# Performance work log

Measured on AMD Instinct MI355X. Metric: run time of the kernel, lower is better.

The kernel has to match this reference:

```python
import jax, jax.numpy as jnp
import numpy as np
import math

D_MODEL = 1024
N_HEADS = 16
D_K = D_MODEL // N_HEADS
MAX_REL = 128


def setup_inputs() -> dict:
    key = jax.random.key(0)
    ks = jax.random.split(key, 10)
    B, S = 2, 2048
    std = 1.0 / math.sqrt(D_MODEL)
    inp = {
        "x": jax.random.normal(ks[0], (B, S, D_MODEL), dtype=jnp.float32),
        "Wq": jax.random.normal(ks[1], (D_MODEL, D_MODEL), dtype=jnp.float32) * std,
        "bq": jnp.zeros((D_MODEL,), dtype=jnp.float32),
        "Wk": jax.random.normal(ks[2], (D_MODEL, D_MODEL), dtype=jnp.float32) * std,
        "bk": jnp.zeros((D_MODEL,), dtype=jnp.float32),
        "Wv": jax.random.normal(ks[3], (D_MODEL, D_MODEL), dtype=jnp.float32) * std,
        "bv": jnp.zeros((D_MODEL,), dtype=jnp.float32),
        "Wo": jax.random.normal(ks[4], (D_MODEL, D_MODEL), dtype=jnp.float32) * std,
        "bo": jnp.zeros((D_MODEL,), dtype=jnp.float32),
        "rel_bias": jax.random.normal(ks[5], (N_HEADS, 2 * MAX_REL + 1), dtype=jnp.float32) * 0.02,
    }
    return inp


def _rel_bias_matrix(rel_bias, seq_len):
    # (H, S, S) gathered relative-position bias
    pos = jnp.arange(seq_len)
    rel = pos[:, None] - pos[None, :]
    idx = jnp.clip(rel, -MAX_REL, MAX_REL) + MAX_REL  # (S, S) in [0, 2M]
    return rel_bias[:, idx]  # (H, S, S)


def reference(x, Wq, bq, Wk, bk, Wv, bv, Wo, bo, rel_bias):
    B, S, _ = x.shape
    def proj(W, b):
        y = x @ W.T + b  # torch Linear: x @ W^T + b
        return y.reshape(B, S, N_HEADS, D_K).transpose(0, 2, 1, 3)  # (B,H,S,Dk)
    Q, K, V = proj(Wq, bq), proj(Wk, bk), proj(Wv, bv)
    scores = jnp.einsum("bhqd,bhkd->bhqk", Q, K) / math.sqrt(D_K)
    scores = scores + _rel_bias_matrix(rel_bias, S)[None]
    attn = jax.nn.softmax(scores, axis=-1)
    out = jnp.einsum("bhqk,bhkd->bhqd", attn, V)
    out = out.transpose(0, 2, 1, 3).reshape(B, S, D_MODEL)
    return out @ Wo.T + bo
```

## Files before the change

### kernel.cpp

```cpp
#include <hip/hip_runtime.h>

static constexpr int DM = 1024;
static constexpr int NH = 16;
static constexpr int DK = 64;
static constexpr int S  = 2048;
static constexpr int B  = 2;
static constexpr float LOG2E = 1.4426950408889634f;
static constexpr float FMAX  = 11.0f;

typedef _Float16 f16;
typedef _Float16 f16x8 __attribute__((ext_vector_type(8)));
typedef _Float16 f16x4 __attribute__((ext_vector_type(4)));
typedef float    f32x4 __attribute__((ext_vector_type(4)));

static constexpr size_t NX = (size_t)B * S * DM;
static constexpr size_t NW = (size_t)DM * DM;

__global__ __launch_bounds__(256) void cvt_f16(const float* __restrict__ x,
                                               const float* __restrict__ wq,
                                               const float* __restrict__ wk,
                                               const float* __restrict__ wv,
                                               const float* __restrict__ wo,
                                               f16* __restrict__ xh,
                                               f16* __restrict__ wqh,
                                               f16* __restrict__ wkh,
                                               f16* __restrict__ wvh,
                                               f16* __restrict__ woh)
{
    const size_t base = ((size_t)blockIdx.x * 256 + threadIdx.x) * 8;
    const float* src; f16* dst; size_t off;
    if (base < NX) { src = x; dst = xh; off = base; }
    else {
        const size_t rem = base - NX;
        const int seg = (int)(rem >> 20);
        off = rem & (NW - 1);
        src = seg == 0 ? wq : (seg == 1 ? wk : (seg == 2 ? wv : wo));
        dst = seg == 0 ? wqh : (seg == 1 ? wkh : (seg == 2 ? wvh : woh));
    }
    float4 a = *(const float4*)&src[off];
    float4 b = *(const float4*)&src[off + 4];
    f16x8 h = { (f16)a.x, (f16)a.y, (f16)a.z, (f16)a.w,
                (f16)b.x, (f16)b.y, (f16)b.z, (f16)b.w };
    *(f16x8*)&dst[off] = h;
}

template<int MODE>
__global__ __launch_bounds__(256) void gemm_h(const f16* __restrict__ A,
                                              const f16* __restrict__ W0,
                                              const f16* __restrict__ W1,
                                              const f16* __restrict__ W2,
                                              const float* __restrict__ b0,
                                              const float* __restrict__ b1,
                                              const float* __restrict__ b2,
                                              void* __restrict__ o0,
                                              void* __restrict__ o1,
                                              void* __restrict__ o2)
{
    __shared__ f16 As[128 * 72];
    __shared__ f16 Bs[128 * 72];

    const int t    = threadIdx.x;
    const int w    = t >> 6;
    const int lane = t & 63;
    const int tx   = lane & 15;
    const int quad = lane >> 4;
    const int wm   = w >> 1;
    const int wn   = w & 1;
    const int m0   = blockIdx.y * 128;

    const f16* W; const float* bias; f16* outh = nullptr; float* outf = nullptr;
    float scale; int n0;
    if (MODE == 0) {
        const int wsel = blockIdx.x >> 3;
        n0   = (blockIdx.x & 7) * 128;
        W    = wsel == 0 ? W0 : (wsel == 1 ? W1 : W2);
        bias = wsel == 0 ? b0 : (wsel == 1 ? b1 : b2);
        outh = (f16*)(wsel == 0 ? o0 : (wsel == 1 ? o1 : o2));
        scale = wsel == 0 ? LOG2E * 0.125f : 1.0f;
    } else {
        n0 = blockIdx.x * 128;
        W = W0; bias = b0; outf = (float*)o0; scale = 1.0f;
    }

    const int lr = t >> 2;
    const int lc = (t & 3) * 8;

    f32x4 acc[4][4];
#pragma unroll
    for (int mt = 0; mt < 4; ++mt)
#pragma unroll
        for (int nt = 0; nt < 4; ++nt) acc[mt][nt] = (f32x4){0.f, 0.f, 0.f, 0.f};

    f16x8 ga[4], gb[4];
    {
        const f16* Ap = A + (size_t)(m0 + lr) * DM + lc;
        const f16* Wp = W + (size_t)(n0 + lr) * DM + lc;
        ga[0] = *(const f16x8*)(Ap);
        ga[1] = *(const f16x8*)(Ap + 32);
        ga[2] = *(const f16x8*)(Ap + (size_t)64 * DM);
        ga[3] = *(const f16x8*)(Ap + (size_t)64 * DM + 32);
        gb[0] = *(const f16x8*)(Wp);
        gb[1] = *(const f16x8*)(Wp + 32);
        gb[2] = *(const f16x8*)(Wp + (size_t)64 * DM);
        gb[3] = *(const f16x8*)(Wp + (size_t)64 * DM + 32);
    }

    for (int k0 = 0; k0 < DM; k0 += 64) {
        __syncthreads();
        *(f16x8*)&As[ lr       * 72 + lc     ] = ga[0];
        *(f16x8*)&As[ lr       * 72 + lc + 32] = ga[1];
        *(f16x8*)&As[(lr + 64) * 72 + lc     ] = ga[2];
        *(f16x8*)&As[(lr + 64) * 72 + lc + 32] = ga[3];
        *(f16x8*)&Bs[ lr       * 72 + lc     ] = gb[0];
        *(f16x8*)&Bs[ lr       * 72 + lc + 32] = gb[1];
        *(f16x8*)&Bs[(lr + 64) * 72 + lc     ] = gb[2];
        *(f16x8*)&Bs[(lr + 64) * 72 + lc + 32] = gb[3];
        if (k0 + 64 < DM) {
            const f16* Ap = A + (size_t)(m0 + lr) * DM + k0 + 64 + lc;
            const f16* Wp = W + (size_t)(n0 + lr) * DM + k0 + 64 + lc;
            ga[0] = *(const f16x8*)(Ap);
            ga[1] = *(const f16x8*)(Ap + 32);
            ga[2] = *(const f16x8*)(Ap + (size_t)64 * DM);
            ga[3] = *(const f16x8*)(Ap + (size_t)64 * DM + 32);
            gb[0] = *(const f16x8*)(Wp);
            gb[1] = *(const f16x8*)(Wp + 32);
            gb[2] = *(const f16x8*)(Wp + (size_t)64 * DM);
            gb[3] = *(const f16x8*)(Wp + (size_t)64 * DM + 32);
        }
        __syncthreads();

        f16x8 af[4][2];
#pragma unroll
        for (int mt = 0; mt < 4; ++mt)
#pragma unroll
            for (int ks = 0; ks < 2; ++ks)
                af[mt][ks] = *(const f16x8*)&As[(wm*64 + mt*16 + tx)*72 + ks*32 + quad*8];
#pragma unroll
        for (int nt = 0; nt < 4; ++nt) {
#pragma unroll
            for (int ks = 0; ks < 2; ++ks) {
                f16x8 bf = *(const f16x8*)&Bs[(wn*64 + nt*16 + tx)*72 + ks*32 + quad*8];
#pragma unroll
                for (int mt = 0; mt < 4; ++mt)
                    acc[mt][nt] = __builtin_amdgcn_mfma_f32_16x16x32_f16(af[mt][ks], bf, acc[mt][nt], 0, 0, 0);
            }
        }
    }

#pragma unroll
    for (int nt = 0; nt < 4; ++nt) {
        const int n = n0 + wn*64 + nt*16 + tx;
        const float bn = bias[n];
#pragma unroll
        for (int mt = 0; mt < 4; ++mt)
#pragma unroll
            for (int r = 0; r < 4; ++r) {
                const int m = m0 + wm*64 + mt*16 + quad*4 + r;
                const float v = (acc[mt][nt][r] + bn) * scale;
                if (MODE == 0) {
                    const int bi = m >> 11;
                    const int ss = m & (S - 1);
                    const int h  = n >> 6;
                    const int dk = n & (DK - 1);
                    outh[((size_t)((bi*NH + h)*S + ss))*DK + dk] = (f16)v;
                } else {
                    outf[(size_t)m * DM + n] = v;
                }
            }
    }
}

__global__ __launch_bounds__(256, 4) void attn_v5(const f16* __restrict__ Q,
                                                  const f16* __restrict__ K,
                                                  const f16* __restrict__ V,
                                                  const float* __restrict__ relb,
                                                  float* __restrict__ On,
                                                  float* __restrict__ lp)
{
    __shared__ f16 Ks[64*72];
    __shared__ f16 Vt[64*72];
    __shared__ float rb2[257];

    const int t    = threadIdx.x;
    const int w    = t >> 6;
    const int lane = t & 63;
    const int tx   = lane & 15;
    const int quad = lane >> 4;
    const int qt   = blockIdx.x >> 1;
    const int sp   = blockIdx.x & 1;
    const int h    = blockIdx.y;
    const int b    = blockIdx.z;
    const int q0   = qt * 128;

    const f16* Qb = Q + (size_t)((b*NH + h) * S) * DK;
    const f16* Kb = K + (size_t)((b*NH + h) * S) * DK;
    const f16* Vb = V + (size_t)((b*NH + h) * S) * DK;

    for (int i = t; i < 257; i += 256) rb2[i] = relb[h*257 + i] * LOG2E - FMAX;

    const int qrow = q0 + w*32 + tx;
    f16x8 qf[2][2];
#pragma unroll
    for (int qb = 0; qb < 2; ++qb)
#pragma unroll
        for (int ks = 0; ks < 2; ++ks)
            qf[qb][ks] = *(const f16x8*)(Qb + (size_t)(qrow + qb*16)*DK + ks*32 + quad*8);

    const f16 onev = (f16)(tx == 0 ? 1.0f : 0.0f);
    const f16x4 af1 = {onev, onev, onev, onev};

    f32x4 oT[4][2];
    f32x4 lacc[2] = {(f32x4){0.f,0.f,0.f,0.f}, (f32x4){0.f,0.f,0.f,0.f}};
#pragma unroll
    for (int d = 0; d < 4; ++d)
#pragma unroll
        for (int qb = 0; qb < 2; ++qb) oT[d][qb] = (f32x4){0.f, 0.f, 0.f, 0.f};

    const int seq = t & 63, d0k = (t >> 6) * 16;
    const int s2 = (t & 31) * 2, d0v = (t >> 5) * 8;
    const int g = ((s2 >> 2) & 3)*16 + (s2 >> 4)*4 + (s2 & 3);

    const int kt0 = sp * (S/128);
    f16x8 kr0, kr1, vr0, vr1;
    {
        const int k0 = kt0 * 64;
        kr0 = *(const f16x8*)(Kb + (size_t)(k0 + seq)*DK + d0k);
        kr1 = *(const f16x8*)(Kb + (size_t)(k0 + seq)*DK + d0k + 8);
        vr0 = *(const f16x8*)(Vb + (size_t)(k0 + s2    )*DK + d0v);
        vr1 = *(const f16x8*)(Vb + (size_t)(k0 + s2 + 1)*DK + d0v);
    }

    for (int kt = kt0; kt < kt0 + S/128; ++kt) {
        const int k0 = kt * 64;

        __syncthreads();
        *(f16x8*)&Ks[seq*72 + d0k    ] = kr0;
        *(f16x8*)&Ks[seq*72 + d0k + 8] = kr1;
        {
            const unsigned int* w0 = (const unsigned int*)&vr0;
            const unsigned int* w1 = (const unsigned int*)&vr1;
#pragma unroll
            for (int jd = 0; jd < 4; ++jd) {
                unsigned int pl = __builtin_amdgcn_perm(w1[jd], w0[jd], 0x05040100u);
                unsigned int ph = __builtin_amdgcn_perm(w1[jd], w0[jd], 0x07060302u);
                *(unsigned int*)&Vt[(d0v + 2*jd    )*72 + g] = pl;
                *(unsigned int*)&Vt[(d0v + 2*jd + 1)*72 + g] = ph;
            }
        }
        if (kt + 1 < kt0 + S/128) {
            const int k0n = k0 + 64;
            kr0 = *(const f16x8*)(Kb + (size_t)(k0n + seq)*DK + d0k);
            kr1 = *(const f16x8*)(Kb + (size_t)(k0n + seq)*DK + d0k + 8);
            vr0 = *(const f16x8*)(Vb + (size_t)(k0n + s2    )*DK + d0v);
            vr1 = *(const f16x8*)(Vb + (size_t)(k0n + s2 + 1)*DK + d0v);
        }
        __syncthreads();

        const bool farlo = (k0 - q0) >= 256;
        const bool farhi = (q0 - k0) >= 192;

        f16x4 pf[4][2];
        if (farlo | farhi) {
            const float bconst = farlo ? rb2[0] : rb2[256];
            const f32x4 bc4 = {bconst, bconst, bconst, bconst};
#pragma unroll
            for (int sb = 0; sb < 4; ++sb) {
                f16x8 kf0 = *(const f16x8*)&Ks[(sb*16 + tx)*72      + quad*8];
                f16x8 kf1 = *(const f16x8*)&Ks[(sb*16 + tx)*72 + 32 + quad*8];
#pragma unroll
                for (int qb = 0; qb < 2; ++qb) {
                    f32x4 sT = __builtin_amdgcn_mfma_f32_16x16x32_f16(kf0, qf[qb][0], bc4, 0, 0, 0);
                    sT       = __builtin_amdgcn_mfma_f32_16x16x32_f16(kf1, qf[qb][1], sT,  0, 0, 0);
#pragma unroll
                    for (int r = 0; r < 4; ++r)
                        pf[sb][qb][r] = (f16)exp2f(sT[r]);
                    lacc[qb] = __builtin_amdgcn_mfma_f32_16x16x16f16(af1, pf[sb][qb], lacc[qb], 0, 0, 0);
                }
            }
        } else {
            const int relbase = qrow - (k0 + quad*4);
            const f32x4 z4 = {0.f, 0.f, 0.f, 0.f};
#pragma unroll
            for (int sb = 0; sb < 4; ++sb) {
                f16x8 kf0 = *(const f16x8*)&Ks[(sb*16 + tx)*72      + quad*8];
                f16x8 kf1 = *(const f16x8*)&Ks[(sb*16 + tx)*72 + 32 + quad*8];
#pragma unroll
                for (int qb = 0; qb < 2; ++qb) {
                    f32x4 sT = __builtin_amdgcn_mfma_f32_16x16x32_f16(kf0, qf[qb][0], z4, 0, 0, 0);
                    sT       = __builtin_amdgcn_mfma_f32_16x16x32_f16(kf1, qf[qb][1], sT, 0, 0, 0);
#pragma unroll
                    for (int r = 0; r < 4; ++r) {
                        int rel = relbase + qb*16 - sb*16 - r;
                        rel = rel < -128 ? -128 : (rel > 128 ? 128 : rel);
                        pf[sb][qb][r] = (f16)exp2f(sT[r] + rb2[rel + 128]);
                    }
                    lacc[qb] = __builtin_amdgcn_mfma_f32_16x16x16f16(af1, pf[sb][qb], lacc[qb], 0, 0, 0);
                }
            }
        }

        __builtin_amdgcn_s_setprio(1);
#pragma unroll
        for (int d = 0; d < 4; ++d) {
#pragma unroll
            for (int sp2 = 0; sp2 < 2; ++sp2) {
                f16x8 vv = *(const f16x8*)&Vt[(d*16 + tx)*72 + quad*16 + sp2*8];
                f16x4 vlo = __builtin_shufflevector(vv, vv, 0, 1, 2, 3);
                f16x4 vhi = __builtin_shufflevector(vv, vv, 4, 5, 6, 7);
#pragma unroll
                for (int qb = 0; qb < 2; ++qb) {
                    oT[d][qb] = __builtin_amdgcn_mfma_f32_16x16x16f16(vlo, pf[sp2*2    ][qb], oT[d][qb], 0, 0, 0);
                    oT[d][qb] = __builtin_amdgcn_mfma_f32_16x16x16f16(vhi, pf[sp2*2 + 1][qb], oT[d][qb], 0, 0, 0);
                }
            }
        }
        __builtin_amdgcn_s_setprio(0);
    }

#pragma unroll
    for (int qb = 0; qb < 2; ++qb) {
        const int q = q0 + w*32 + qb*16 + tx;
        if (quad == 0)
            lp[(((size_t)sp*B + b)*NH + h)*S + q] = lacc[qb][0];
#pragma unroll
        for (int d = 0; d < 4; ++d)
            *(f32x4*)&On[(size_t)sp*NX + ((size_t)(b*S + q))*DM + h*DK + d*16 + quad*4] = oT[d][qb];
    }
}

__global__ __launch_bounds__(256) void combine(const float* __restrict__ On,
                                               const float* __restrict__ lp,
                                               f16* __restrict__ AOh)
{
    const size_t i8 = ((size_t)blockIdx.x * 256 + threadIdx.x) * 8;
    const int token = (int)(i8 >> 10);
    const int c     = (int)(i8 & (DM - 1));
    const int b     = token >> 11;
    const int st    = token & (S - 1);
    const int h     = c >> 6;
    const float l = lp[((size_t)b*NH + h)*S + st]
                  + lp[(((size_t)B + b)*NH + h)*S + st];
    const float inv = 1.0f / l;
    float4 a0 = *(const float4*)&On[i8];
    float4 a1 = *(const float4*)&On[i8 + 4];
    float4 b0 = *(const float4*)&On[NX + i8];
    float4 b1 = *(const float4*)&On[NX + i8 + 4];
    f16x8 o = { (f16)((a0.x + b0.x) * inv), (f16)((a0.y + b0.y) * inv),
                (f16)((a0.z + b0.z) * inv), (f16)((a0.w + b0.w) * inv),
                (f16)((a1.x + b1.x) * inv), (f16)((a1.y + b1.y) * inv),
                (f16)((a1.z + b1.z) * inv), (f16)((a1.w + b1.w) * inv) };
    *(f16x8*)&AOh[i8] = o;
}

extern "C" void kernel_launch(void* const* d_in, const int* in_sizes, int n_in,
                              void* d_out, int out_size, void* d_ws, size_t ws_size,
                              hipStream_t stream)
{
    const float* x    = (const float*)d_in[0];
    const float* Wq   = (const float*)d_in[1];
    const float* bq   = (const float*)d_in[2];
    const float* Wk   = (const float*)d_in[3];
    const float* bk   = (const float*)d_in[4];
    const float* Wv   = (const float*)d_in[5];
    const float* bv   = (const float*)d_in[6];
    const float* Wo   = (const float*)d_in[7];
    const float* bo   = (const float*)d_in[8];
    const float* relb = (const float*)d_in[9];

    f16* Xh  = (f16*)d_ws;
    f16* Wqh = Xh  + NX;
    f16* Wkh = Wqh + NW;
    f16* Wvh = Wkh + NW;
    f16* Woh = Wvh + NW;
    f16* Qh  = Woh + NW;
    f16* Kh  = Qh  + NX;
    f16* Vh  = Kh  + NX;
    f16* AOh = Vh  + NX;
    float* On = (float*)(AOh + NX);
    float* lpart = On + 2*NX;

    cvt_f16<<<(NX + 4*NW) / (256*8), 256, 0, stream>>>(x, Wq, Wk, Wv, Wo,
                                                       Xh, Wqh, Wkh, Wvh, Woh);
    gemm_h<0><<<dim3(24, 32), 256, 0, stream>>>(Xh, Wqh, Wkh, Wvh,
                                                bq, bk, bv, Qh, Kh, Vh);
    attn_v5<<<dim3((S/128)*2, NH, B), 256, 0, stream>>>(Qh, Kh, Vh, relb, On, lpart);
    combine<<<NX / (256*8), 256, 0, stream>>>(On, lpart, AOh);
    gemm_h<1><<<dim3(8, 32), 256, 0, stream>>>(AOh, Woh, nullptr, nullptr,
                                               bo, nullptr, nullptr,
                                               d_out, nullptr, nullptr);
}
```

Before: 228.1 us.

## Split attention keys four ways, drop register prefetch, sum row totals in scalars

The attention kernel now splits the key range across four blocks per query tile instead of two, and raises the occupancy hint to 8 blocks per CU. The register double-buffered prefetch of the next K/V tile is removed, and the row-sum is accumulated as scalar adds plus a cross-lane shuffle reduction instead of an extra MFMA with a ones vector. The aim is more parallel blocks and lower register pressure. The cost is doubling the fp32 partial-output traffic that the combine kernel must read and reduce, and losing load/compute overlap inside each block.

```diff
diff --git a/kernel.cpp b/kernel.cpp
--- a/kernel.cpp
+++ b/kernel.cpp
@@ -15,6 +15,7 @@
 
 static constexpr size_t NX = (size_t)B * S * DM;
 static constexpr size_t NW = (size_t)DM * DM;
+static constexpr int NSP = 4;
 
 __global__ __launch_bounds__(256) void cvt_f16(const float* __restrict__ x,
                                                const float* __restrict__ wq,
@@ -170,7 +171,7 @@
     }
 }
 
-__global__ __launch_bounds__(256, 4) void attn_v5(const f16* __restrict__ Q,
+__global__ __launch_bounds__(256, 8) void attn_v7(const f16* __restrict__ Q,
                                                   const f16* __restrict__ K,
                                                   const f16* __restrict__ V,
                                                   const float* __restrict__ relb,
@@ -186,8 +187,8 @@
     const int lane = t & 63;
     const int tx   = lane & 15;
     const int quad = lane >> 4;
-    const int qt   = blockIdx.x >> 1;
-    const int sp   = blockIdx.x & 1;
+    const int qt   = blockIdx.x >> 2;
+    const int sp   = blockIdx.x & 3;
     const int h    = blockIdx.y;
     const int b    = blockIdx.z;
     const int q0   = qt * 128;
@@ -206,37 +207,29 @@
         for (int ks = 0; ks < 2; ++ks)
             qf[qb][ks] = *(const f16x8*)(Qb + (size_t)(qrow + qb*16)*DK + ks*32 + quad*8);
 
-    const f16 onev = (f16)(tx == 0 ? 1.0f : 0.0f);
-    const f16x4 af1 = {onev, onev, onev, onev};
-
     f32x4 oT[4][2];
-    f32x4 lacc[2] = {(f32x4){0.f,0.f,0.f,0.f}, (f32x4){0.f,0.f,0.f,0.f}};
+    float lsum[2] = {0.f, 0.f};
 #pragma unroll
     for (int d = 0; d < 4; ++d)
 #pragma unroll
         for (int qb = 0; qb < 2; ++qb) oT[d][qb] = (f32x4){0.f, 0.f, 0.f, 0.f};
 
-    const int seq = t & 63, d0k = (t >> 6) * 16;
-    const int s2 = (t & 31) * 2, d0v = (t >> 5) * 8;
-    const int g = ((s2 >> 2) & 3)*16 + (s2 >> 4)*4 + (s2 & 3);
-
-    const int kt0 = sp * (S/128);
-    f16x8 kr0, kr1, vr0, vr1;
-    {
-        const int k0 = kt0 * 64;
-        kr0 = *(const f16x8*)(Kb + (size_t)(k0 + seq)*DK + d0k);
-        kr1 = *(const f16x8*)(Kb + (size_t)(k0 + seq)*DK + d0k + 8);
-        vr0 = *(const f16x8*)(Vb + (size_t)(k0 + s2    )*DK + d0v);
-        vr1 = *(const f16x8*)(Vb + (size_t)(k0 + s2 + 1)*DK + d0v);
-    }
-
-    for (int kt = kt0; kt < kt0 + S/128; ++kt) {
+    const int kt0 = sp * (S/64/NSP);
+    for (int kt = kt0; kt < kt0 + S/64/NSP; ++kt) {
         const int k0 = kt * 64;
+
+        const int seq = t & 63, d0k = (t >> 6) * 16;
+        f16x8 kr0 = *(const f16x8*)(Kb + (size_t)(k0 + seq)*DK + d0k);
+        f16x8 kr1 = *(const f16x8*)(Kb + (size_t)(k0 + seq)*DK + d0k + 8);
+        const int s2 = (t & 31) * 2, d0v = (t >> 5) * 8;
+        f16x8 vr0 = *(const f16x8*)(Vb + (size_t)(k0 + s2    )*DK + d0v);
+        f16x8 vr1 = *(const f16x8*)(Vb + (size_t)(k0 + s2 + 1)*DK + d0v);
 
         __syncthreads();
         *(f16x8*)&Ks[seq*72 + d0k    ] = kr0;
         *(f16x8*)&Ks[seq*72 + d0k + 8] = kr1;
         {
+            const int g = ((s2 >> 2) & 3)*16 + (s2 >> 4)*4 + (s2 & 3);
             const unsigned int* w0 = (const unsigned int*)&vr0;
             const unsigned int* w1 = (const unsigned int*)&vr1;
 #pragma unroll
@@ -247,13 +240,6 @@
                 *(unsigned int*)&Vt[(d0v + 2*jd + 1)*72 + g] = ph;
             }
         }
-        if (kt + 1 < kt0 + S/128) {
-            const int k0n = k0 + 64;
-            kr0 = *(const f16x8*)(Kb + (size_t)(k0n + seq)*DK + d0k);
-            kr1 = *(const f16x8*)(Kb + (size_t)(k0n + seq)*DK + d0k + 8);
-            vr0 = *(const f16x8*)(Vb + (size_t)(k0n + s2    )*DK + d0v);
-            vr1 = *(const f16x8*)(Vb + (size_t)(k0n + s2 + 1)*DK + d0v);
-        }
         __syncthreads();
 
         const bool farlo = (k0 - q0) >= 256;
@@ -272,9 +258,11 @@
                     f32x4 sT = __builtin_amdgcn_mfma_f32_16x16x32_f16(kf0, qf[qb][0], bc4, 0, 0, 0);
                     sT       = __builtin_amdgcn_mfma_f32_16x16x32_f16(kf1, qf[qb][1], sT,  0, 0, 0);
 #pragma unroll
-                    for (int r = 0; r < 4; ++r)
-                        pf[sb][qb][r] = (f16)exp2f(sT[r]);
-                    lacc[qb] = __builtin_amdgcn_mfma_f32_16x16x16f16(af1, pf[sb][qb], lacc[qb], 0, 0, 0);
+                    for (int r = 0; r < 4; ++r) {
+                        const float p = exp2f(sT[r]);
+                        lsum[qb] += p;
+                        pf[sb][qb][r] = (f16)p;
+                    }
                 }
             }
         } else {
@@ -292,9 +280,10 @@
                     for (int r = 0; r < 4; ++r) {
                         int rel = relbase + qb*16 - sb*16 - r;
                         rel = rel < -128 ? -128 : (rel > 128 ? 128 : rel);
-                        pf[sb][qb][r] = (f16)exp2f(sT[r] + rb2[rel + 128]);
+                        const float p = exp2f(sT[r] + rb2[rel + 128]);
+                        lsum[qb] += p;
+                        pf[sb][qb][r] = (f16)p;
                     }
-                    lacc[qb] = __builtin_amdgcn_mfma_f32_16x16x16f16(af1, pf[sb][qb], lacc[qb], 0, 0, 0);
                 }
             }
         }
@@ -319,9 +308,12 @@
 
 #pragma unroll
     for (int qb = 0; qb < 2; ++qb) {
+        float l = lsum[qb];
+        l += __shfl_xor(l, 16);
+        l += __shfl_xor(l, 32);
         const int q = q0 + w*32 + qb*16 + tx;
         if (quad == 0)
-            lp[(((size_t)sp*B + b)*NH + h)*S + q] = lacc[qb][0];
+            lp[(((size_t)sp*B + b)*NH + h)*S + q] = l;
 #pragma unroll
         for (int d = 0; d < 4; ++d)
             *(f32x4*)&On[(size_t)sp*NX + ((size_t)(b*S + q))*DM + h*DK + d*16 + quad*4] = oT[d][qb];
@@ -338,17 +330,23 @@
     const int b     = token >> 11;
     const int st    = token & (S - 1);
     const int h     = c >> 6;
-    const float l = lp[((size_t)b*NH + h)*S + st]
-                  + lp[(((size_t)B + b)*NH + h)*S + st];
+    float l = 0.f;
+#pragma unroll
+    for (int s4 = 0; s4 < NSP; ++s4)
+        l += lp[(((size_t)s4*B + b)*NH + h)*S + st];
     const float inv = 1.0f / l;
-    float4 a0 = *(const float4*)&On[i8];
-    float4 a1 = *(const float4*)&On[i8 + 4];
-    float4 b0 = *(const float4*)&On[NX + i8];
-    float4 b1 = *(const float4*)&On[NX + i8 + 4];
-    f16x8 o = { (f16)((a0.x + b0.x) * inv), (f16)((a0.y + b0.y) * inv),
-                (f16)((a0.z + b0.z) * inv), (f16)((a0.w + b0.w) * inv),
-                (f16)((a1.x + b1.x) * inv), (f16)((a1.y + b1.y) * inv),
-                (f16)((a1.z + b1.z) * inv), (f16)((a1.w + b1.w) * inv) };
+    float4 a0 = {0.f,0.f,0.f,0.f}, a1 = {0.f,0.f,0.f,0.f};
+#pragma unroll
+    for (int s4 = 0; s4 < NSP; ++s4) {
+        float4 x0 = *(const float4*)&On[(size_t)s4*NX + i8];
+        float4 x1 = *(const float4*)&On[(size_t)s4*NX + i8 + 4];
+        a0.x += x0.x; a0.y += x0.y; a0.z += x0.z; a0.w += x0.w;
+        a1.x += x1.x; a1.y += x1.y; a1.z += x1.z; a1.w += x1.w;
+    }
+    f16x8 o = { (f16)(a0.x * inv), (f16)(a0.y * inv),
+                (f16)(a0.z * inv), (f16)(a0.w * inv),
+                (f16)(a1.x * inv), (f16)(a1.y * inv),
+                (f16)(a1.z * inv), (f16)(a1.w * inv) };
     *(f16x8*)&AOh[i8] = o;
 }
 
@@ -377,13 +375,13 @@
     f16* Vh  = Kh  + NX;
     f16* AOh = Vh  + NX;
     float* On = (float*)(AOh + NX);
-    float* lpart = On + 2*NX;
+    float* lpart = On + (size_t)NSP*NX;
 
     cvt_f16<<<(NX + 4*NW) / (256*8), 256, 0, stream>>>(x, Wq, Wk, Wv, Wo,
                                                        Xh, Wqh, Wkh, Wvh, Woh);
     gemm_h<0><<<dim3(24, 32), 256, 0, stream>>>(Xh, Wqh, Wkh, Wvh,
                                                 bq, bk, bv, Qh, Kh, Vh);
-    attn_v5<<<dim3((S/128)*2, NH, B), 256, 0, stream>>>(Qh, Kh, Vh, relb, On, lpart);
+    attn_v7<<<dim3((S/128)*NSP, NH, B), 256, 0, stream>>>(Qh, Kh, Vh, relb, On, lpart);
     combine<<<NX / (256*8), 256, 0, stream>>>(On, lpart, AOh);
     gemm_h<1><<<dim3(8, 32), 256, 0, stream>>>(AOh, Woh, nullptr, nullptr,
                                                bo, nullptr, nullptr,
```

Measured after the change: 426.7 us. 1.87x slower.
